# Performance work log

Measured on AMD Instinct MI355X. Metric: run time of the kernel, lower is better.

## Reference

```python
import jax, jax.numpy as jnp
import numpy as np

EPS = 1e-6

def elu_plus_one(x):
    # F.elu(x) + 1 == exp(x) for x<=0, x+1 for x>0
    return jnp.where(x > 0, x + 1.0, jnp.exp(jnp.minimum(x, 0.0)))

def setup_inputs() -> dict:
    key = jax.random.key(0)
    k1, k2, k3, k4, k5 = jax.random.split(key, 5)
    B, S, D, M = 2, 4096, 1024, 4
    queries = jax.random.normal(k1, (B, S, D), dtype=jnp.float32)
    keys = jax.random.normal(k2, (B, S, D), dtype=jnp.float32)
    values = jax.random.normal(k3, (B, S, D), dtype=jnp.float32)
    # small-scale warm memory state; norms positive (accumulated sigma(k) sums)
    memories = jax.random.normal(k4, (M, D, D), dtype=jnp.float32) * 0.02
    memory_norms = jax.random.uniform(k5, (M, D), dtype=jnp.float32)
    return {"queries": queries, "keys": keys, "values": values,
            "memories": memories, "memory_norms": memory_norms}

def reference(queries, keys, values, memories, memory_norms):
    B, S, D = queries.shape
    M = memories.shape[0]

    # ---------------- retrieve ----------------
    sigma_q = elu_plus_one(queries)                                   # (B,S,D)
    a_mem = jnp.einsum('bsd,mde->mbse', sigma_q, memories)            # (M,B,S,D)
    qnorm = jnp.einsum('bsd,md->mbs', sigma_q, memory_norms)          # (M,B,S)
    outputs = a_mem / jnp.clip(qnorm, EPS, None)[..., None]           # (M,B,S,D)
    # relevance: sigma(Q) @ landmark, mean over seq -> (M,B)
    rel = qnorm.mean(axis=-1)
    empty = jnp.sum(jnp.abs(memory_norms), axis=1) < EPS              # (M,)
    NEG = jnp.float32(-1e30)
    rel = jnp.where(empty[:, None], NEG, rel)
    weights = jax.nn.softmax(rel, axis=0)                             # (M,B)
    outputs = jnp.where(empty[:, None, None, None], 0.0, outputs)
    out = jnp.einsum('mbsd,mb->bsd', outputs, weights)
    # if every slot empty, torch returns zeros
    out = jnp.where(jnp.all(empty), jnp.zeros_like(out), out)

    # ---------------- update (delta rule, current_idx = 0) ----------------
    sigma_k = elu_plus_one(keys)                                      # (B,S,D)
    mem0, norm0 = memories[0], memory_norms[0]
    retrieved_unnorm = jnp.matmul(sigma_k, mem0)                      # (B,S,D)
    knorm = jnp.clip(jnp.matmul(sigma_k, norm0), EPS, None)[..., None]
    delta_v = values - retrieved_unnorm / knorm
    mem_update = jnp.einsum('bsd,bse->de', sigma_k, delta_v) / (B * S)
    new_memory = jax.lax.stop_gradient(mem0 + mem_update)             # .detach()
    new_memory_norm = jax.lax.stop_gradient(norm0 + sigma_k.sum(axis=(0, 1)) / B)
    return out, new_memory, new_memory_norm
```

## Files before the change

### kernel.cpp

```cpp
#include <hip/hip_runtime.h>
#include <math.h>

#define B_ 2
#define S_ 4096
#define D_ 1024
#define M_ 4
#define N_ (B_*S_)
#define EPS 1e-6f

typedef unsigned short u16;
typedef __bf16 bf16x8 __attribute__((ext_vector_type(8)));
typedef float  f32x4  __attribute__((ext_vector_type(4)));

__device__ __forceinline__ float elu1(float x) {
    return x > 0.0f ? x + 1.0f : __expf(x);
}

__device__ __forceinline__ u16 f2b(float f) {
    unsigned int u = __float_as_uint(f);
    return (u16)((u + 0x7FFFu + ((u >> 16) & 1u)) >> 16);
}

#define GLDS16(gp, lp) __builtin_amdgcn_global_load_lds( \
    (const __attribute__((address_space(1))) void*)(gp), \
    (__attribute__((address_space(3))) void*)(lp), 16, 0, 0)

__global__ __launch_bounds__(256) void k1_stats(
    const float* __restrict__ Q, const float* __restrict__ mnorm,
    float* __restrict__ qnorm,
    u16* __restrict__ sQ,
    float* __restrict__ knorm, float* __restrict__ colsum)
{
    int r = blockIdx.x;
    int t = threadIdx.x;
    if (r < 32) {
        knorm[r * 256 + t] = 0.0f;
        if (r < 4) colsum[r * 256 + t] = 0.0f;
    }
    float4 q4 = *(const float4*)(Q + (size_t)r * D_ + t * 4);
    float sq0 = elu1(q4.x), sq1 = elu1(q4.y), sq2 = elu1(q4.z), sq3 = elu1(q4.w);

    uint2 sv;
    sv.x = (unsigned)f2b(sq0) | ((unsigned)f2b(sq1) << 16);
    sv.y = (unsigned)f2b(sq2) | ((unsigned)f2b(sq3) << 16);
    *(uint2*)(sQ + (size_t)r * D_ + t * 4) = sv;

    float vals[M_];
    #pragma unroll
    for (int m = 0; m < M_; ++m) {
        float4 w4 = *(const float4*)(mnorm + m * D_ + t * 4);
        vals[m] = sq0 * w4.x + sq1 * w4.y + sq2 * w4.z + sq3 * w4.w;
    }

    __shared__ float sbuf[M_][4];
    int wave = t >> 6, lane = t & 63;
    #pragma unroll
    for (int i = 0; i < M_; ++i) {
        float v = vals[i];
        #pragma unroll
        for (int off = 32; off > 0; off >>= 1) v += __shfl_down(v, off, 64);
        if (lane == 0) sbuf[i][wave] = v;
    }
    __syncthreads();
    if (t == 0) {
        #pragma unroll
        for (int m = 0; m < M_; ++m)
            qnorm[(size_t)m * N_ + r] = sbuf[m][0] + sbuf[m][1] + sbuf[m][2] + sbuf[m][3];
    }
}

__global__ __launch_bounds__(256) void prep_k(
    const float* __restrict__ K, const float* __restrict__ mnorm,
    u16* __restrict__ sk, u16* __restrict__ skT,
    float* __restrict__ colsum, float* __restrict__ knorm)
{
    __shared__ float tile[64][65];
    __shared__ float mn0[64];
    int r0 = blockIdx.x * 64;
    int d0 = blockIdx.y * 64;
    int t = threadIdx.x;
    int rr = t >> 4, c4 = (t & 15) * 4;
    if (t >= 128 && t < 192) mn0[t - 128] = mnorm[d0 + (t - 128)];
    #pragma unroll
    for (int i = 0; i < 4; ++i) {
        int rri = rr + i * 16;
        float4 k4 = *(const float4*)(K + (size_t)(r0 + rri) * D_ + d0 + c4);
        float e0 = elu1(k4.x), e1 = elu1(k4.y), e2 = elu1(k4.z), e3 = elu1(k4.w);
        uint2 v; v.x = (unsigned)f2b(e0) | ((unsigned)f2b(e1) << 16);
        v.y = (unsigned)f2b(e2) | ((unsigned)f2b(e3) << 16);
        *(uint2*)(sk + (size_t)(r0 + rri) * D_ + d0 + c4) = v;
        tile[rri][c4 + 0] = e0; tile[rri][c4 + 1] = e1;
        tile[rri][c4 + 2] = e2; tile[rri][c4 + 3] = e3;
    }
    __syncthreads();
    #pragma unroll
    for (int i = 0; i < 4; ++i) {
        int dd = rr + i * 16;
        float v0 = tile[c4 + 0][dd], v1 = tile[c4 + 1][dd];
        float v2 = tile[c4 + 2][dd], v3 = tile[c4 + 3][dd];
        uint2 v; v.x = (unsigned)f2b(v0) | ((unsigned)f2b(v1) << 16);
        v.y = (unsigned)f2b(v2) | ((unsigned)f2b(v3) << 16);
        *(uint2*)(skT + (size_t)(d0 + dd) * N_ + r0 + c4) = v;
    }
    if (t < 64) {
        float s = 0.0f;
        #pragma unroll
        for (int j = 0; j < 64; ++j) s += tile[t][j] * mn0[j];
        atomicAdd(&knorm[r0 + t], s);
    } else if (t < 128) {
        int c = t - 64;
        float s = 0.0f;
        #pragma unroll
        for (int j = 0; j < 64; ++j) s += tile[j][c];
        atomicAdd(&colsum[d0 + c], s);
    }
}

__global__ __launch_bounds__(256) void prep_memT(
    const float* __restrict__ Mem, u16* __restrict__ MemT,
    float* __restrict__ out_mem)
{
    __shared__ float tile[64][65];
    int m = blockIdx.z;
    int e0 = blockIdx.x * 64, d0 = blockIdx.y * 64;
    int t = threadIdx.x, rr = t >> 4, c4 = (t & 15) * 4;
    #pragma unroll
    for (int i = 0; i < 4; ++i) {
        int dd = rr + i * 16;
        float4 v4 = *(const float4*)(Mem + ((size_t)m * D_ + d0 + dd) * D_ + e0 + c4);
        tile[dd][c4 + 0] = v4.x; tile[dd][c4 + 1] = v4.y;
        tile[dd][c4 + 2] = v4.z; tile[dd][c4 + 3] = v4.w;
        if (m == 0)
            *(float4*)(out_mem + (size_t)(d0 + dd) * D_ + e0 + c4) = v4;
    }
    __syncthreads();
    #pragma unroll
    for (int i = 0; i < 4; ++i) {
        int ee = rr + i * 16;
        float v0 = tile[c4 + 0][ee], v1 = tile[c4 + 1][ee];
        float v2 = tile[c4 + 2][ee], v3 = tile[c4 + 3][ee];
        uint2 v; v.x = (unsigned)f2b(v0) | ((unsigned)f2b(v1) << 16);
        v.y = (unsigned)f2b(v2) | ((unsigned)f2b(v3) << 16);
        *(uint2*)(MemT + (size_t)(e0 + ee) * (M_ * D_) + m * D_ + d0 + c4) = v;
    }
}

__global__ __launch_bounds__(512) void k2_weights(
    const float* __restrict__ mnorm, const float* __restrict__ qnorm,
    float* __restrict__ weights)
{
    __shared__ float sbuf[12][8];
    int t = threadIdx.x, wave = t >> 6, lane = t & 63;
    float vals[12];
    #pragma unroll
    for (int m = 0; m < M_; ++m) {
        float v = 0.0f;
        for (int d = t; d < D_; d += 512) v += fabsf(mnorm[m * D_ + d]);
        vals[m] = v;
    }
    #pragma unroll
    for (int mb = 0; mb < M_ * B_; ++mb) {
        int m = mb >> 1, b = mb & 1;
        const float4* p = (const float4*)(qnorm + (size_t)m * N_ + (size_t)b * S_);
        float v = 0.0f;
        for (int i = t; i < S_ / 4; i += 512) {
            float4 x = p[i];
            v += x.x + x.y + x.z + x.w;
        }
        vals[4 + mb] = v;
    }
    #pragma unroll
    for (int i = 0; i < 12; ++i) {
        float v = vals[i];
        #pragma unroll
        for (int off = 32; off > 0; off >>= 1) v += __shfl_down(v, off, 64);
        if (lane == 0) sbuf[i][wave] = v;
    }
    __syncthreads();
    if (t == 0) {
        bool empty[M_]; bool all_empty = true;
        float relsum[M_ * B_];
        #pragma unroll
        for (int m = 0; m < M_; ++m) {
            float sa = 0.0f;
            #pragma unroll
            for (int w = 0; w < 8; ++w) sa += sbuf[m][w];
            empty[m] = (sa < EPS);
            all_empty = all_empty && empty[m];
        }
        #pragma unroll
        for (int mb = 0; mb < M_ * B_; ++mb) {
            float sv = 0.0f;
            #pragma unroll
            for (int w = 0; w < 8; ++w) sv += sbuf[4 + mb][w];
            relsum[mb] = sv;
        }
        for (int b = 0; b < B_; ++b) {
            float rel[M_]; float mx = -3.0e38f;
            #pragma unroll
            for (int m = 0; m < M_; ++m) {
                rel[m] = empty[m] ? -1.0e30f : relsum[m * B_ + b] * (1.0f / (float)S_);
                mx = fmaxf(mx, rel[m]);
            }
            float se = 0.0f;
            #pragma unroll
            for (int m = 0; m < M_; ++m) { rel[m] = __expf(rel[m] - mx); se += rel[m]; }
            #pragma unroll
            for (int m = 0; m < M_; ++m) {
                float wv = rel[m] / se;
                if (empty[m] || all_empty) wv = 0.0f;
                weights[m * B_ + b] = wv;
            }
        }
    }
}

__global__ __launch_bounds__(256) void k2_cvec(
    const float* __restrict__ qnorm, const float* __restrict__ weights,
    const float* __restrict__ mnorm, const float* __restrict__ colsum,
    float* __restrict__ ratT, float* __restrict__ norm_out)
{
    int g = blockIdx.x * 256 + threadIdx.x;
    if (g < N_) {
        int b = g / S_;
        float cs[M_];
        #pragma unroll
        for (int m = 0; m < M_; ++m)
            cs[m] = fmaxf(weights[m * B_ + b] / fmaxf(qnorm[(size_t)m * N_ + g], EPS), 1e-20f);
        ratT[0 * (size_t)N_ + g] = cs[0] / cs[1];
        ratT[1 * (size_t)N_ + g] = cs[1] / cs[2];
        ratT[2 * (size_t)N_ + g] = cs[2] / cs[3];
        ratT[3 * (size_t)N_ + g] = cs[3];
    }
    if (g < D_) norm_out[g] = mnorm[g] + colsum[g] * (1.0f / (float)B_);
}

__device__ __forceinline__ void tile_mma(
    const u16* Asb, const u16* Bsb, int aoff, int boff, f32x4 (&acc)[4][4])
{
    bf16x8 af[4], bf[4];
    #pragma unroll
    for (int i = 0; i < 4; ++i) {
        af[i] = *(const bf16x8*)((const char*)Asb + aoff + i * 1024);
        bf[i] = *(const bf16x8*)((const char*)Bsb + boff + i * 1024);
    }
    #pragma unroll
    for (int mi = 0; mi < 4; ++mi)
        #pragma unroll
        for (int ni = 0; ni < 4; ++ni)
            acc[mi][ni] = __builtin_amdgcn_mfma_f32_16x16x32_bf16(
                af[mi], bf[ni], acc[mi][ni], 0, 0, 0);
}

__device__ __forceinline__ void gemm_seg(
    u16* As, u16* Bs,
    const u16* __restrict__ A, int lda, int ak0,
    const u16* __restrict__ B, int ldb, int bk0,
    int rb, int cb, int klen,
    f32x4 (&acc)[4][4])
{
    const int tid  = threadIdx.x;
    const int lane = tid & 63;
    const int wid  = tid >> 6;
    const int wr   = wid >> 1, wc = wid & 1;
    const int r15  = lane & 15;

    const int srow0 = (wid * 2 + 0) * 16 + (lane >> 2);
    const int srow1 = (wid * 2 + 1) * 16 + (lane >> 2);
    const int sg    = ((lane & 3) ^ ((lane >> 3) & 3)) * 8;
    const u16* Ag0 = A + (size_t)(rb + srow0) * lda + ak0 + sg;
    const u16* Ag1 = A + (size_t)(rb + srow1) * lda + ak0 + sg;
    const u16* Bg0 = B + (size_t)(cb + srow0) * ldb + bk0 + sg;
    const u16* Bg1 = B + (size_t)(cb + srow1) * ldb + bk0 + sg;
    const int lo0 = (wid * 2 + 0) * 512;
    const int lo1 = (wid * 2 + 1) * 512;

    const int xo   = (((lane >> 4) ^ ((r15 >> 1) & 3)) * 16);
    const int aoff = (wr * 64 + r15) * 64 + xo;
    const int boff = (wc * 64 + r15) * 64 + xo;

    GLDS16(Ag0, As + lo0);
    GLDS16(Ag1, As + lo1);
    GLDS16(Bg0, Bs + lo0);
    GLDS16(Bg1, Bs + lo1);
    asm volatile("s_waitcnt vmcnt(0)" ::: "memory");
    __builtin_amdgcn_s_barrier();

    int cur = 0;
    for (int kt = 32; kt < klen; kt += 32) {
        int nxt = cur ^ 1;
        GLDS16(Ag0 + kt, As + nxt * 4096 + lo0);
        GLDS16(Ag1 + kt, As + nxt * 4096 + lo1);
        GLDS16(Bg0 + kt, Bs + nxt * 4096 + lo0);
        GLDS16(Bg1 + kt, Bs + nxt * 4096 + lo1);
        tile_mma(As + cur * 4096, Bs + cur * 4096, aoff, boff, acc);
        asm volatile("s_waitcnt vmcnt(0) lgkmcnt(0)" ::: "memory");
        __builtin_amdgcn_s_barrier();
        cur = nxt;
    }
    tile_mma(As + cur * 4096, Bs + cur * 4096, aoff, boff, acc);
    asm volatile("s_waitcnt lgkmcnt(0)" ::: "memory");
    __builtin_amdgcn_s_barrier();
}

__device__ __forceinline__ void epi_out(
    f32x4 (&acc)[4][4], float* __restrict__ out, int rb, int cb)
{
    int lane = threadIdx.x & 63, wid = threadIdx.x >> 6;
    int wr = wid >> 1, wc = wid & 1, r15 = lane & 15;
    #pragma unroll
    for (int mi = 0; mi < 4; ++mi) {
        int row0 = rb + wr * 64 + mi * 16 + (lane >> 4) * 4;
        #pragma unroll
        for (int ni = 0; ni < 4; ++ni) {
            int col = cb + wc * 64 + ni * 16 + r15;
            #pragma unroll
            for (int r = 0; r < 4; ++r)
                out[(size_t)(row0 + r) * D_ + col] = acc[mi][ni][r];
        }
    }
}

__device__ __forceinline__ void epi_delta(
    f32x4 (&acc)[4][4], const float* __restrict__ V,
    const float* __restrict__ knorm, u16* __restrict__ deltaT,
    int rb, int cb)
{
    int lane = threadIdx.x & 63, wid = threadIdx.x >> 6;
    int wr = wid >> 1, wc = wid & 1, r15 = lane & 15;
    #pragma unroll
    for (int mi = 0; mi < 4; ++mi) {
        int row0 = rb + wr * 64 + mi * 16 + (lane >> 4) * 4;
        float inv[4];
        #pragma unroll
        for (int r = 0; r < 4; ++r) inv[r] = 1.0f / fmaxf(knorm[row0 + r], EPS);
        #pragma unroll
        for (int ni = 0; ni < 4; ++ni) {
            int col = cb + wc * 64 + ni * 16 + r15;
            float dv[4];
            #pragma unroll
            for (int r = 0; r < 4; ++r)
                dv[r] = V[(size_t)(row0 + r) * D_ + col] - acc[mi][ni][r] * inv[r];
            uint2 pv;
            pv.x = (unsigned)f2b(dv[0]) | ((unsigned)f2b(dv[1]) << 16);
            pv.y = (unsigned)f2b(dv[2]) | ((unsigned)f2b(dv[3]) << 16);
            *(uint2*)(deltaT + (size_t)col * N_ + row0) = pv;
        }
    }
}

__global__ __launch_bounds__(256, 4) void g34_fused(
    const u16* __restrict__ sQ, const u16* __restrict__ MemT,
    const u16* __restrict__ sk, const float* __restrict__ V,
    const float* __restrict__ knorm, const float* __restrict__ ratT,
    float* __restrict__ out, u16* __restrict__ deltaT)
{
    __shared__ u16 As[2 * 4096];
    __shared__ u16 Bs[2 * 4096];
    int hw = blockIdx.x;
    int x   = hw & 7;
    int l   = hw >> 3;
    int z   = l >> 6;
    int idx = l & 63;
    int by  = x * 8 + (idx >> 3);
    int bx  = idx & 7;
    int rb = by * 128, cb = bx * 128;
    int lane = threadIdx.x & 63, wid = threadIdx.x >> 6;
    int wr = wid >> 1;
    f32x4 acc[4][4];
    #pragma unroll
    for (int i = 0; i < 4; ++i)
        #pragma unroll
        for (int j = 0; j < 4; ++j) {
            f32x4 zz = {0.0f, 0.0f, 0.0f, 0.0f};
            acc[i][j] = zz;
        }
    if (z == 0) {
        #pragma unroll 1
        for (int m = 0; m < M_; ++m) {
            gemm_seg(As, Bs, sQ, D_, 0, MemT, M_ * D_, m * D_, rb, cb, D_, acc);
            const float* rp = ratT + (size_t)m * N_;
            #pragma unroll
            for (int mi = 0; mi < 4; ++mi) {
                int row0 = rb + wr * 64 + mi * 16 + (lane >> 4) * 4;
                float4 rt = *(const float4*)(rp + row0);
                #pragma unroll
                for (int ni = 0; ni < 4; ++ni) {
                    acc[mi][ni][0] *= rt.x; acc[mi][ni][1] *= rt.y;
                    acc[mi][ni][2] *= rt.z; acc[mi][ni][3] *= rt.w;
                }
            }
        }
        epi_out(acc, out, rb, cb);
    } else {
        gemm_seg(As, Bs, sk, D_, 0, MemT, M_ * D_, 0, rb, cb, D_, acc);
        epi_delta(acc, V, knorm, deltaT, rb, cb);
    }
}

#define KSPLIT 8
__global__ __launch_bounds__(256, 4) void g5_update(
    const u16* __restrict__ skT, const u16* __restrict__ deltaT,
    float* __restrict__ memout)
{
    __shared__ u16 As[2 * 4096];
    __shared__ u16 Bs[2 * 4096];
    f32x4 acc[4][4];
    #pragma unroll
    for (int i = 0; i < 4; ++i)
        #pragma unroll
        for (int j = 0; j < 4; ++j) {
            f32x4 zz = {0.0f, 0.0f, 0.0f, 0.0f};
            acc[i][j] = zz;
        }
    int rb = blockIdx.y * 128, cb = blockIdx.x * 128;
    int k0 = blockIdx.z * (N_ / KSPLIT);
    gemm_seg(As, Bs, skT, N_, k0, deltaT, N_, k0, rb, cb, N_ / KSPLIT, acc);
    int lane = threadIdx.x & 63, wid = threadIdx.x >> 6;
    int wr = wid >> 1, wc = wid & 1, r15 = lane & 15;
    const float sc = 1.0f / (float)N_;
    #pragma unroll
    for (int mi = 0; mi < 4; ++mi) {
        int row0 = rb + wr * 64 + mi * 16 + (lane >> 4) * 4;
        #pragma unroll
        for (int ni = 0; ni < 4; ++ni) {
            int col = cb + wc * 64 + ni * 16 + r15;
            #pragma unroll
            for (int r = 0; r < 4; ++r)
                atomicAdd(memout + (size_t)(row0 + r) * D_ + col, acc[mi][ni][r] * sc);
        }
    }
}

extern "C" void kernel_launch(void* const* d_in, const int* in_sizes, int n_in,
                              void* d_out, int out_size, void* d_ws, size_t ws_size,
                              hipStream_t stream) {
    const float* Q     = (const float*)d_in[0];
    const float* K     = (const float*)d_in[1];
    const float* V     = (const float*)d_in[2];
    const float* Mem   = (const float*)d_in[3];
    const float* Mnorm = (const float*)d_in[4];

    float* out      = (float*)d_out;
    float* out_mem  = out + (size_t)N_ * D_;
    float* out_norm = out_mem + (size_t)D_ * D_;

    char* wsb = (char*)d_ws;
    float* qnorm   = (float*)wsb;
    float* knorm   = qnorm + (size_t)M_ * N_;
    float* colsum  = knorm + N_;
    float* weights = colsum + D_;
    float* ratT    = weights + M_ * B_;
    u16* MemT   = (u16*)(wsb + (size_t)1  * (1 << 20));
    u16* sk     = (u16*)(wsb + (size_t)9  * (1 << 20));
    u16* skT    = (u16*)(wsb + (size_t)25 * (1 << 20));
    u16* sQ     = (u16*)(wsb + (size_t)41 * (1 << 20));
    u16* deltaT = (u16*)(wsb + (size_t)57 * (1 << 20));

    hipLaunchKernelGGL(k1_stats, dim3(N_), dim3(256), 0, stream, Q, Mnorm, qnorm, sQ, knorm, colsum);
    hipLaunchKernelGGL(prep_k, dim3(128, 16), dim3(256), 0, stream, K, Mnorm, sk, skT, colsum, knorm);
    hipLaunchKernelGGL(prep_memT, dim3(16, 16, 4), dim3(256), 0, stream, Mem, MemT, out_mem);
    hipLaunchKernelGGL(k2_weights, dim3(1), dim3(512), 0, stream, Mnorm, qnorm, weights);
    hipLaunchKernelGGL(k2_cvec, dim3(32), dim3(256), 0, stream, qnorm, weights, Mnorm, colsum, ratT, out_norm);
    hipLaunchKernelGGL(g34_fused, dim3(1024), dim3(256), 0, stream,
                       sQ, MemT, sk, V, knorm, ratT, out, deltaT);
    hipLaunchKernelGGL(g5_update, dim3(8, 8, KSPLIT), dim3(256), 0, stream, skT, deltaT, out_mem);
}
```

Baseline: 200.7 us.

## Triple-buffer GEMM k-loop with one barrier per step and remap update grid

Replaces the double-buffered LDS pipeline in the shared GEMM segment with a three-stage ring that prefetches two k-tiles ahead. Each iteration now uses a partial vmcnt wait and a single barrier before compute, which lets global-to-LDS loads overlap more with MFMA work. Shared memory per block grows by half and launch bounds drop from 4 to 3 blocks per CU, so occupancy falls. The update kernel also moves to a 1D grid whose block order puts the K-split index in the low bits, which changes L2 locality and the pattern of atomic contention.

New measurement: 203.7 us. No clear change (+1.5%).

```diff
diff --git a/kernel.cpp b/kernel.cpp
--- a/kernel.cpp
+++ b/kernel.cpp
@@ -279,26 +279,35 @@
     const int aoff = (wr * 64 + r15) * 64 + xo;
     const int boff = (wc * 64 + r15) * 64 + xo;
 
+    const int nt = klen >> 5;
+
     GLDS16(Ag0, As + lo0);
     GLDS16(Ag1, As + lo1);
     GLDS16(Bg0, Bs + lo0);
     GLDS16(Bg1, Bs + lo1);
+    GLDS16(Ag0 + 32, As + 4096 + lo0);
+    GLDS16(Ag1 + 32, As + 4096 + lo1);
+    GLDS16(Bg0 + 32, Bs + 4096 + lo0);
+    GLDS16(Bg1 + 32, Bs + 4096 + lo1);
+
+    int bcur = 0;
+    for (int t = 0; t < nt - 1; ++t) {
+        asm volatile("s_waitcnt vmcnt(4)" ::: "memory");
+        __builtin_amdgcn_s_barrier();
+        if (t + 2 < nt) {
+            int bn = bcur ? bcur - 1 : 2;
+            int kt = (t + 2) << 5;
+            GLDS16(Ag0 + kt, As + bn * 4096 + lo0);
+            GLDS16(Ag1 + kt, As + bn * 4096 + lo1);
+            GLDS16(Bg0 + kt, Bs + bn * 4096 + lo0);
+            GLDS16(Bg1 + kt, Bs + bn * 4096 + lo1);
+        }
+        tile_mma(As + bcur * 4096, Bs + bcur * 4096, aoff, boff, acc);
+        bcur = (bcur + 1 == 3) ? 0 : bcur + 1;
+    }
     asm volatile("s_waitcnt vmcnt(0)" ::: "memory");
     __builtin_amdgcn_s_barrier();
-
-    int cur = 0;
-    for (int kt = 32; kt < klen; kt += 32) {
-        int nxt = cur ^ 1;
-        GLDS16(Ag0 + kt, As + nxt * 4096 + lo0);
-        GLDS16(Ag1 + kt, As + nxt * 4096 + lo1);
-        GLDS16(Bg0 + kt, Bs + nxt * 4096 + lo0);
-        GLDS16(Bg1 + kt, Bs + nxt * 4096 + lo1);
-        tile_mma(As + cur * 4096, Bs + cur * 4096, aoff, boff, acc);
-        asm volatile("s_waitcnt vmcnt(0) lgkmcnt(0)" ::: "memory");
-        __builtin_amdgcn_s_barrier();
-        cur = nxt;
-    }
-    tile_mma(As + cur * 4096, Bs + cur * 4096, aoff, boff, acc);
+    tile_mma(As + bcur * 4096, Bs + bcur * 4096, aoff, boff, acc);
     asm volatile("s_waitcnt lgkmcnt(0)" ::: "memory");
     __builtin_amdgcn_s_barrier();
 }
@@ -349,14 +358,14 @@
     }
 }
 
-__global__ __launch_bounds__(256, 4) void g34_fused(
+__global__ __launch_bounds__(256, 3) void g34_fused(
     const u16* __restrict__ sQ, const u16* __restrict__ MemT,
     const u16* __restrict__ sk, const float* __restrict__ V,
     const float* __restrict__ knorm, const float* __restrict__ ratT,
     float* __restrict__ out, u16* __restrict__ deltaT)
 {
-    __shared__ u16 As[2 * 4096];
-    __shared__ u16 Bs[2 * 4096];
+    __shared__ u16 As[3 * 4096];
+    __shared__ u16 Bs[3 * 4096];
     int hw = blockIdx.x;
     int x   = hw & 7;
     int l   = hw >> 3;
@@ -399,12 +408,12 @@
 }
 
 #define KSPLIT 8
-__global__ __launch_bounds__(256, 4) void g5_update(
+__global__ __launch_bounds__(256, 3) void g5_update(
     const u16* __restrict__ skT, const u16* __restrict__ deltaT,
     float* __restrict__ memout)
 {
-    __shared__ u16 As[2 * 4096];
-    __shared__ u16 Bs[2 * 4096];
+    __shared__ u16 As[3 * 4096];
+    __shared__ u16 Bs[3 * 4096];
     f32x4 acc[4][4];
     #pragma unroll
     for (int i = 0; i < 4; ++i)
@@ -413,8 +422,12 @@
             f32x4 zz = {0.0f, 0.0f, 0.0f, 0.0f};
             acc[i][j] = zz;
         }
-    int rb = blockIdx.y * 128, cb = blockIdx.x * 128;
-    int k0 = blockIdx.z * (N_ / KSPLIT);
+    int hw = blockIdx.x;
+    int kz = hw & 7;
+    int l  = hw >> 3;
+    int by = l >> 3, bx = l & 7;
+    int rb = by * 128, cb = bx * 128;
+    int k0 = kz * (N_ / KSPLIT);
     gemm_seg(As, Bs, skT, N_, k0, deltaT, N_, k0, rb, cb, N_ / KSPLIT, acc);
     int lane = threadIdx.x & 63, wid = threadIdx.x >> 6;
     int wr = wid >> 1, wc = wid & 1, r15 = lane & 15;
@@ -464,5 +477,5 @@
     hipLaunchKernelGGL(k2_cvec, dim3(32), dim3(256), 0, stream, qnorm, weights, Mnorm, colsum, ratT, out_norm);
     hipLaunchKernelGGL(g34_fused, dim3(1024), dim3(256), 0, stream,
                        sQ, MemT, sk, V, knorm, ratT, out, deltaT);
-    hipLaunchKernelGGL(g5_update, dim3(8, 8, KSPLIT), dim3(256), 0, stream, skT, deltaT, out_mem);
-}
+    hipLaunchKernelGGL(g5_update, dim3(512), dim3(256), 0, stream, skT, deltaT, out_mem);
+}
```
